# Performance work log

Hardware: AMD Instinct MI355X
Metric: run time of the kernel (lower is better)

The kernel has to match this reference:

```python
import jax, jax.numpy as jnp
import numpy as np

HIDDEN_DIM = 256
N = 8192


def setup_inputs() -> dict:
    key = jax.random.key(0)
    k1, k2, k3, k4 = jax.random.split(key, 4)
    img = jax.random.normal(k1, (N, HIDDEN_DIM), dtype=jnp.float32)
    text = jax.random.normal(k2, (N, HIDDEN_DIM), dtype=jnp.float32)
    # nn.Linear(hidden_dim, hidden_dim, bias=False) weights, shape [out, in]
    scale = 1.0 / np.sqrt(HIDDEN_DIM)
    Wq = jax.random.uniform(k3, (HIDDEN_DIM, HIDDEN_DIM), dtype=jnp.float32, minval=-scale, maxval=scale)
    Wk = jax.random.uniform(k4, (HIDDEN_DIM, HIDDEN_DIM), dtype=jnp.float32, minval=-scale, maxval=scale)
    return {"img": img, "text": text, "Wq": Wq, "Wk": Wk}


def reference(img, text, Wq, Wk):
    d = img.shape[-1]
    norm_fact = 1.0 / jnp.sqrt(jnp.asarray(d, dtype=img.dtype))
    Q = img @ Wq.T                       # [N, D]
    K = text @ Wk.T                      # [N, D]
    scores = Q @ K.T                     # [N, N]
    # softmax over dim=1 (keys), then scaled by 1/sqrt(D)
    attn = jax.nn.softmax(scores, axis=1) * norm_fact
    out_img = attn @ img                 # [N, D]
    out_text = attn @ text               # [N, D]
    return (out_img, out_text)
```

## Files before the change

### kernel.cpp

```cpp
#include <hip/hip_runtime.h>

typedef unsigned short ushort_t;
typedef unsigned int uint_t;
typedef __attribute__((ext_vector_type(8))) short short8;
typedef __attribute__((ext_vector_type(8))) _Float16 half8;
typedef __attribute__((ext_vector_type(4))) float float4v;

#define MFMA_BF16(a, b, c) __builtin_amdgcn_mfma_f32_16x16x32_bf16((a), (b), (c), 0, 0, 0)
#define MFMA_F16(a, b, c) __builtin_amdgcn_mfma_f32_16x16x32_f16((a), (b), (c), 0, 0, 0)

#define NQ 8192
#define DIM 256
#define DV 512

__device__ __forceinline__ ushort_t f2bf(float x) {
  union { float f; uint_t u; } v; v.f = x;
  return (ushort_t)((v.u + 0x7fffu + ((v.u >> 16) & 1u)) >> 16);
}
__device__ __forceinline__ float bf2f(ushort_t b) {
  union { uint_t u; float f; } v; v.u = ((uint_t)b) << 16;
  return v.f;
}

__device__ __forceinline__ half8 cvt8h(const float* p) {
  float4v a = *(const float4v*)p;
  float4v b = *(const float4v*)(p + 4);
  half8 r;
  r[0] = (_Float16)a[0]; r[1] = (_Float16)a[1];
  r[2] = (_Float16)a[2]; r[3] = (_Float16)a[3];
  r[4] = (_Float16)b[0]; r[5] = (_Float16)b[1];
  r[6] = (_Float16)b[2]; r[7] = (_Float16)b[3];
  return r;
}

__device__ __forceinline__ half8 as_h8(short8 s) {
  union { short8 s; half8 h; } u; u.s = s; return u.h;
}

__device__ __forceinline__ void load_lds_16(const void* g, void* l) {
  __builtin_amdgcn_global_load_lds(
      (const __attribute__((address_space(1))) uint_t*)g,
      (__attribute__((address_space(3))) uint_t*)l, 16, 0, 0);
}

__global__ __launch_bounds__(256, 2) void proj_kernel(
    const float* __restrict__ img, const float* __restrict__ text,
    const float* __restrict__ Wq, const float* __restrict__ Wk,
    _Float16* __restrict__ Qh, _Float16* __restrict__ Kh) {
  const int lane = threadIdx.x & 63;
  const int wv = threadIdx.x >> 6;
  const int l16 = lane & 15;
  const int quad = lane >> 4;
  const float* A = blockIdx.z ? text : img;
  const float* W = blockIdx.z ? Wk : Wq;
  _Float16* C = blockIdx.z ? Kh : Qh;
  const int row = blockIdx.x * 64 + wv * 16 + l16;
  const int colbase = blockIdx.y * 64;

  float4v acc[4];
#pragma unroll
  for (int c = 0; c < 4; ++c) acc[c] = (float4v){0.f, 0.f, 0.f, 0.f};

#pragma unroll
  for (int f = 0; f < 8; ++f) {
    const int k0 = f * 32 + quad * 8;
    half8 af = cvt8h(A + (size_t)row * DIM + k0);
#pragma unroll
    for (int c = 0; c < 4; ++c) {
      half8 bfr = cvt8h(W + (size_t)(colbase + c * 16 + l16) * DIM + k0);
      acc[c] = MFMA_F16(af, bfr, acc[c]);
    }
  }
  const int rbase = blockIdx.x * 64 + wv * 16 + quad * 4;
#pragma unroll
  for (int c = 0; c < 4; ++c)
#pragma unroll
    for (int r = 0; r < 4; ++r)
      C[(size_t)(rbase + r) * DIM + colbase + c * 16 + l16] = (_Float16)acc[c][r];
}

__global__ __launch_bounds__(256) void make_vt_kernel(
    const float* __restrict__ img, const float* __restrict__ text,
    ushort_t* __restrict__ Vt) {
  __shared__ float tile[64][65];
  const int n0 = blockIdx.x * 64;
  const int c0 = blockIdx.y * 64;
  const float* src = (c0 < 256) ? img : text;
  const int cc0 = (c0 < 256) ? c0 : (c0 - 256);
  const int tid = threadIdx.x;

#pragma unroll
  for (int i = 0; i < 4; ++i) {
    const int r = i * 16 + (tid >> 4);
    const int c = (tid & 15) * 4;
    *(float4v*)&tile[r][c] = *(const float4v*)(src + (size_t)(n0 + r) * DIM + cc0 + c);
  }
  __syncthreads();
  const int c = tid >> 2;
  const int seg = tid & 3;
  ushort_t tmp[16];
#pragma unroll
  for (int t = 0; t < 16; ++t) tmp[t] = f2bf(tile[seg * 16 + t][c]);
  ushort_t* dst = Vt + (size_t)(c0 + c) * NQ + n0 + seg * 16;
  *(short8*)dst = *(short8*)&tmp[0];
  *(short8*)(dst + 8) = *(short8*)&tmp[8];
}

__global__ __launch_bounds__(256, 2) void attn_kernel(
    const _Float16* __restrict__ Qh, const _Float16* __restrict__ Kh,
    const ushort_t* __restrict__ Vt, float* __restrict__ pacc,
    float* __restrict__ pdenom, int kps, int swz) {
  __shared__ __align__(16) ushort_t ldsK[32 * DIM];
  __shared__ __align__(16) ushort_t ldsV[DV * 32];
  __shared__ __align__(16) ushort_t ldsP[64 * 32];

  const int tid = threadIdx.x;
  const int lane = tid & 63;
  const int wv = tid >> 6;
  const int l16 = lane & 15;
  const int quad = lane >> 4;
  const int id = blockIdx.x;
  int qtile, split;
  if (swz) {
    split = (id & 7) >> 1;
    qtile = ((id >> 3) << 1) | (id & 1);
  } else {
    split = id >> 7;
    qtile = id & 127;
  }
  const int kbeg = split * kps;
  const int sw2 = (l16 >> 1) & 3;

  short8 qf[8];
  {
    const _Float16* qptr = Qh + (size_t)(qtile * 64 + wv * 16 + l16) * DIM;
#pragma unroll
    for (int f = 0; f < 8; ++f)
      qf[f] = *(const short8*)(qptr + f * 32 + quad * 8);
  }

  float4v acc[4][8];
#pragma unroll
  for (int m = 0; m < 4; ++m)
#pragma unroll
    for (int c = 0; c < 8; ++c) acc[m][c] = (float4v){0.f, 0.f, 0.f, 0.f};
  float dacc[4] = {0.f, 0.f, 0.f, 0.f};

  const int ntiles = kps >> 5;
  for (int it = 0; it < ntiles; ++it) {
    const int k0 = kbeg + it * 32;
    __syncthreads();
#pragma unroll
    for (int i = 0; i < 4; ++i) {
      const int chunk = i * 256 + tid;
      const int n = chunk >> 5;
      const int cs = (chunk & 31) ^ (n & 7);
      load_lds_16(Kh + (size_t)(k0 + n) * DIM + cs * 8,
                  (char*)ldsK + (i * 256 + wv * 64) * 16);
    }
#pragma unroll
    for (int i = 0; i < 8; ++i) {
      const int chunk = i * 256 + tid;
      const int vrow = chunk >> 2;
      const int dc = (chunk & 3) ^ ((vrow >> 1) & 3);
      load_lds_16(Vt + (size_t)vrow * NQ + k0 + dc * 8,
                  (char*)ldsV + (i * 256 + wv * 64) * 16);
    }
    __syncthreads();

    float4v s0 = (float4v){0.f, 0.f, 0.f, 0.f};
    float4v s1 = (float4v){0.f, 0.f, 0.f, 0.f};
    const int swk = l16 & 7;
#pragma unroll
    for (int f = 0; f < 8; ++f) {
      const int cs = ((f * 4 + quad) ^ swk) * 8;
      short8 kb0 = *(const short8*)(ldsK + l16 * DIM + cs);
      short8 kb1 = *(const short8*)(ldsK + (l16 + 16) * DIM + cs);
      s0 = MFMA_F16(as_h8(qf[f]), as_h8(kb0), s0);
      s1 = MFMA_F16(as_h8(qf[f]), as_h8(kb1), s1);
    }

    ushort_t pb0[4], pb1[4];
#pragma unroll
    for (int r = 0; r < 4; ++r) {
      pb0[r] = f2bf(__expf(s0[r]));
      pb1[r] = f2bf(__expf(s1[r]));
    }
#pragma unroll
    for (int r = 0; r < 4; ++r) {
      float t = bf2f(pb0[r]) + bf2f(pb1[r]);
      t += __shfl_xor(t, 1);
      t += __shfl_xor(t, 2);
      t += __shfl_xor(t, 4);
      t += __shfl_xor(t, 8);
      dacc[r] += t;
    }
#pragma unroll
    for (int r = 0; r < 4; ++r) {
      const int rb = wv * 16 + quad * 4 + r;
      const int swp = (rb >> 1) & 3;
      ldsP[rb * 32 + ((l16 >> 3) ^ swp) * 8 + (l16 & 7)] = pb0[r];
      ldsP[rb * 32 + ((2 + (l16 >> 3)) ^ swp) * 8 + (l16 & 7)] = pb1[r];
    }
    __syncthreads();

    short8 pa[4];
#pragma unroll
    for (int m = 0; m < 4; ++m)
      pa[m] = *(const short8*)(ldsP + (m * 16 + l16) * 32 + (quad ^ sw2) * 8);
#pragma unroll
    for (int c = 0; c < 8; ++c) {
      const int vcol = (wv * 8 + c) * 16 + l16;
      short8 vb = *(const short8*)(ldsV + vcol * 32 + (quad ^ sw2) * 8);
#pragma unroll
      for (int m = 0; m < 4; ++m)
        acc[m][c] = MFMA_BF16(pa[m], vb, acc[m][c]);
    }
  }

  float* pout = pacc + (size_t)split * ((size_t)NQ * DV);
#pragma unroll
  for (int m = 0; m < 4; ++m) {
    const int rowbase = qtile * 64 + m * 16 + quad * 4;
#pragma unroll
    for (int c = 0; c < 8; ++c) {
      const int col = (wv * 8 + c) * 16 + l16;
#pragma unroll
      for (int r = 0; r < 4; ++r)
        pout[(size_t)(rowbase + r) * DV + col] = acc[m][c][r];
    }
  }
  if (l16 == 0) {
    const int rowbase = qtile * 64 + wv * 16 + quad * 4;
#pragma unroll
    for (int r = 0; r < 4; ++r)
      pdenom[split * NQ + rowbase + r] = dacc[r];
  }
}

__global__ __launch_bounds__(256) void combine_kernel(
    const float* __restrict__ pacc, const float* __restrict__ pdenom,
    float* __restrict__ out, int ks) {
  const int idx = blockIdx.x * 256 + threadIdx.x;
  const int n = idx >> 7;
  const int c4 = (idx & 127) << 2;
  float4v s = (float4v){0.f, 0.f, 0.f, 0.f};
  float d = 0.f;
  for (int sp = 0; sp < ks; ++sp) {
    s += *(const float4v*)(pacc + (size_t)sp * ((size_t)NQ * DV) + (size_t)n * DV + c4);
    d += pdenom[sp * NQ + n];
  }
  const float scale = 1.0f / (16.0f * d);
  s *= scale;
  float* dst = (c4 < 256) ? (out + (size_t)n * DIM + c4)
                          : (out + (size_t)NQ * DIM + (size_t)n * DIM + (c4 - 256));
  *(float4v*)dst = s;
}

extern "C" void kernel_launch(void* const* d_in, const int* in_sizes, int n_in,
                              void* d_out, int out_size, void* d_ws, size_t ws_size,
                              hipStream_t stream) {
  const float* img = (const float*)d_in[0];
  const float* text = (const float*)d_in[1];
  const float* Wq = (const float*)d_in[2];
  const float* Wk = (const float*)d_in[3];
  float* out = (float*)d_out;
  char* ws = (char*)d_ws;

  _Float16* Qh = (_Float16*)ws;
  _Float16* Kh = (_Float16*)(ws + ((size_t)4 << 20));
  ushort_t* Vt = (ushort_t*)(ws + ((size_t)8 << 20));
  const size_t accsz = (size_t)NQ * DV * sizeof(float);
  const size_t base = (size_t)16 << 20;

  int ks = 4;
  if (ws_size < base + 4 * (accsz + NQ * sizeof(float))) ks = 2;
  if (ws_size < base + 2 * (accsz + NQ * sizeof(float))) ks = 1;
  float* pacc = (float*)(ws + base);
  float* pdenom = (float*)(ws + base + (size_t)ks * accsz);
  const int swz = (ks == 4) ? 1 : 0;

  hipLaunchKernelGGL(proj_kernel, dim3(128, 4, 2), dim3(256), 0, stream,
                     img, text, Wq, Wk, Qh, Kh);
  hipLaunchKernelGGL(make_vt_kernel, dim3(128, 8), dim3(256), 0, stream,
                     img, text, Vt);
  hipLaunchKernelGGL(attn_kernel, dim3(128 * ks), dim3(256), 0, stream,
                     Qh, Kh, Vt, pacc, pdenom, NQ / ks, swz);
  hipLaunchKernelGGL(combine_kernel, dim3((NQ * DV / 4) / 256), dim3(256), 0, stream,
                     pacc, pdenom, out, ks);
}
```

Baseline: 274.2 us.

## Raise key-split count to eight and store normalized partials in fp16

```diff
diff --git a/kernel.cpp b/kernel.cpp
--- a/kernel.cpp
+++ b/kernel.cpp
@@ -4,6 +4,7 @@
 typedef unsigned int uint_t;
 typedef __attribute__((ext_vector_type(8))) short short8;
 typedef __attribute__((ext_vector_type(8))) _Float16 half8;
+typedef __attribute__((ext_vector_type(4))) _Float16 half4;
 typedef __attribute__((ext_vector_type(4))) float float4v;
 
 #define MFMA_BF16(a, b, c) __builtin_amdgcn_mfma_f32_16x16x32_bf16((a), (b), (c), 0, 0, 0)
@@ -108,8 +109,8 @@
 
 __global__ __launch_bounds__(256, 2) void attn_kernel(
     const _Float16* __restrict__ Qh, const _Float16* __restrict__ Kh,
-    const ushort_t* __restrict__ Vt, float* __restrict__ pacc,
-    float* __restrict__ pdenom, int kps, int swz) {
+    const ushort_t* __restrict__ Vt, _Float16* __restrict__ pacc,
+    float* __restrict__ pdenom, int kps, int ks) {
   __shared__ __align__(16) ushort_t ldsK[32 * DIM];
   __shared__ __align__(16) ushort_t ldsV[DV * 32];
   __shared__ __align__(16) ushort_t ldsP[64 * 32];
@@ -121,7 +122,10 @@
   const int quad = lane >> 4;
   const int id = blockIdx.x;
   int qtile, split;
-  if (swz) {
+  if (ks == 8) {
+    split = id & 7;
+    qtile = id >> 3;
+  } else if (ks == 4) {
     split = (id & 7) >> 1;
     qtile = ((id >> 3) << 1) | (id & 1);
   } else {
@@ -218,16 +222,28 @@
     }
   }
 
-  float* pout = pacc + (size_t)split * ((size_t)NQ * DV);
+  __syncthreads();
+  float* ldsD = (float*)ldsP;
+  if (l16 == 0) {
+#pragma unroll
+    for (int r = 0; r < 4; ++r)
+      ldsD[wv * 16 + quad * 4 + r] = dacc[r];
+  }
+  __syncthreads();
+
+  _Float16* pout = pacc + (size_t)split * ((size_t)NQ * DV);
 #pragma unroll
   for (int m = 0; m < 4; ++m) {
+    float invd[4];
+#pragma unroll
+    for (int r = 0; r < 4; ++r) invd[r] = 1.0f / ldsD[m * 16 + quad * 4 + r];
     const int rowbase = qtile * 64 + m * 16 + quad * 4;
 #pragma unroll
     for (int c = 0; c < 8; ++c) {
       const int col = (wv * 8 + c) * 16 + l16;
 #pragma unroll
       for (int r = 0; r < 4; ++r)
-        pout[(size_t)(rowbase + r) * DV + col] = acc[m][c][r];
+        pout[(size_t)(rowbase + r) * DV + col] = (_Float16)(acc[m][c][r] * invd[r]);
     }
   }
   if (l16 == 0) {
@@ -239,18 +255,23 @@
 }
 
 __global__ __launch_bounds__(256) void combine_kernel(
-    const float* __restrict__ pacc, const float* __restrict__ pdenom,
+    const _Float16* __restrict__ pacc, const float* __restrict__ pdenom,
     float* __restrict__ out, int ks) {
   const int idx = blockIdx.x * 256 + threadIdx.x;
   const int n = idx >> 7;
   const int c4 = (idx & 127) << 2;
   float4v s = (float4v){0.f, 0.f, 0.f, 0.f};
-  float d = 0.f;
+  float dsum = 0.f;
   for (int sp = 0; sp < ks; ++sp) {
-    s += *(const float4v*)(pacc + (size_t)sp * ((size_t)NQ * DV) + (size_t)n * DV + c4);
-    d += pdenom[sp * NQ + n];
-  }
-  const float scale = 1.0f / (16.0f * d);
+    const float d = pdenom[sp * NQ + n];
+    half4 x = *(const half4*)(pacc + (size_t)sp * ((size_t)NQ * DV) + (size_t)n * DV + c4);
+    s[0] += d * (float)x[0];
+    s[1] += d * (float)x[1];
+    s[2] += d * (float)x[2];
+    s[3] += d * (float)x[3];
+    dsum += d;
+  }
+  const float scale = 1.0f / (16.0f * dsum);
   s *= scale;
   float* dst = (c4 < 256) ? (out + (size_t)n * DIM + c4)
                           : (out + (size_t)NQ * DIM + (size_t)n * DIM + (c4 - 256));
@@ -270,22 +291,21 @@
   _Float16* Qh = (_Float16*)ws;
   _Float16* Kh = (_Float16*)(ws + ((size_t)4 << 20));
   ushort_t* Vt = (ushort_t*)(ws + ((size_t)8 << 20));
-  const size_t accsz = (size_t)NQ * DV * sizeof(float);
+  const size_t accsz = (size_t)NQ * DV * sizeof(_Float16);
   const size_t base = (size_t)16 << 20;
 
-  int ks = 4;
+  int ks = 8;
+  if (ws_size < base + 8 * (accsz + NQ * sizeof(float))) ks = 4;
   if (ws_size < base + 4 * (accsz + NQ * sizeof(float))) ks = 2;
-  if (ws_size < base + 2 * (accsz + NQ * sizeof(float))) ks = 1;
-  float* pacc = (float*)(ws + base);
+  _Float16* pacc = (_Float16*)(ws + base);
   float* pdenom = (float*)(ws + base + (size_t)ks * accsz);
-  const int swz = (ks == 4) ? 1 : 0;
 
   hipLaunchKernelGGL(proj_kernel, dim3(128, 4, 2), dim3(256), 0, stream,
                      img, text, Wq, Wk, Qh, Kh);
   hipLaunchKernelGGL(make_vt_kernel, dim3(128, 8), dim3(256), 0, stream,
                      img, text, Vt);
   hipLaunchKernelGGL(attn_kernel, dim3(128 * ks), dim3(256), 0, stream,
-                     Qh, Kh, Vt, pacc, pdenom, NQ / ks, swz);
+                     Qh, Kh, Vt, pacc, pdenom, NQ / ks, ks);
   hipLaunchKernelGGL(combine_kernel, dim3((NQ * DV / 4) / 256), dim3(256), 0, stream,
                      pacc, pdenom, out, ks);
 }
```

Result: slower. 280.6 us (+2.3%).
